# Performance work log

Measured on AMD Instinct MI355X. Metric: run time of the kernel, lower is better.

## Reference

```python
import jax, jax.numpy as jnp
import numpy as np

N = 16384
C = 128
F = 128

def setup_inputs() -> dict:
    key = jax.random.key(0)
    k1, k2, k3, k4 = jax.random.split(key, 4)
    X = jax.random.normal(k1, (N, C), dtype=jnp.float32)
    adj = jax.random.uniform(k2, (N, N), dtype=jnp.float32)
    W = jax.random.normal(k3, (C, F), dtype=jnp.float32) * 0.05
    b = jax.random.normal(k4, (F,), dtype=jnp.float32) * 0.05
    return {"X": X, "adj": adj, "W": W, "b": b}

def reference(X, adj, W, b):
    # adj_hat = adj + I (self-loops)
    adj_hat = adj + jnp.eye(adj.shape[0], dtype=adj.dtype)
    # D^{-1/2}: inverse of sqrt of the diagonal degree matrix == 1/sqrt(rowsum)
    d_inv_sqrt = 1.0 / jnp.sqrt(jnp.sum(adj_hat, axis=1))  # [N]
    # Symmetric normalization via row/col scaling (same math as D^-1/2 @ A @ D^-1/2)
    adj_norm = adj_hat * d_inv_sqrt[:, None] * d_inv_sqrt[None, :]
    # Feature transform first (N*C*F) then aggregate (N*N*F)
    out = adj_norm @ (X @ W) + b
    return jax.nn.relu(out)
```

## Files before the change

### kernel.cpp

```cpp
#include <hip/hip_runtime.h>
#include <hip/hip_bf16.h>

typedef __attribute__((ext_vector_type(8))) short short8;
typedef __attribute__((ext_vector_type(4))) float f32x4;

#define N_NODES 16384
#define FEAT 128
#define NTILES 256
#define KSPLIT 2
#define NT2 (NTILES / KSPLIT)

__device__ __forceinline__ short f2bf(float x) {
  union { float f; unsigned u; } v;
  v.f = x;
  unsigned r = v.u + 0x7fffu + ((v.u >> 16) & 1u);
  return (short)(r >> 16);
}

__global__ __launch_bounds__(256) void rowsum_kernel(
    const float* __restrict__ adj, float* __restrict__ dinv)
{
  const int row = blockIdx.x;
  const float4* p4 = (const float4*)(adj + (size_t)row * N_NODES);
  float s = 0.f;
  #pragma unroll 4
  for (int i = threadIdx.x; i < N_NODES / 4; i += 256) {
    float4 v = p4[i];
    s += (v.x + v.y) + (v.z + v.w);
  }
  #pragma unroll
  for (int off = 32; off > 0; off >>= 1) s += __shfl_down(s, off, 64);
  __shared__ float part[4];
  if ((threadIdx.x & 63) == 0) part[threadIdx.x >> 6] = s;
  __syncthreads();
  if (threadIdx.x == 0) {
    float tot = (part[0] + part[1]) + (part[2] + part[3]) + 1.0f;
    dinv[row] = rsqrtf(tot);
  }
}

__global__ __launch_bounds__(256) void xw_kernel(
    const float* __restrict__ X, const float* __restrict__ W,
    const float* __restrict__ dinv,
    __hip_bfloat16* __restrict__ Ypack)
{
  __shared__ __align__(16) float Ws[64][128];
  __shared__ __align__(16) float Xs[32][128];
  __shared__ __align__(16) short Ts[128][40];
  const int tid = threadIdx.x;
  const int row0 = blockIdx.x << 5;

  {
    const float4* Xg = (const float4*)(X + ((size_t)row0 << 7));
    float4* Xl = (float4*)&Xs[0][0];
    #pragma unroll
    for (int i = 0; i < 4; ++i) Xl[tid + (i << 8)] = Xg[tid + (i << 8)];
  }
  const int f  = tid & 127;
  const int rr = tid >> 7;
  float acc[16];
  #pragma unroll
  for (int k = 0; k < 16; ++k) acc[k] = 0.f;

  for (int cc = 0; cc < 2; ++cc) {
    __syncthreads();
    {
      const float4* Wg = (const float4*)(W + ((size_t)cc << 13));
      float4* Wl = (float4*)&Ws[0][0];
      #pragma unroll
      for (int i = 0; i < 8; ++i) Wl[tid + (i << 8)] = Wg[tid + (i << 8)];
    }
    __syncthreads();
    for (int c4 = 0; c4 < 16; ++c4) {
      const int cl = c4 << 2;
      const float w0 = Ws[cl + 0][f];
      const float w1 = Ws[cl + 1][f];
      const float w2 = Ws[cl + 2][f];
      const float w3 = Ws[cl + 3][f];
      const int cg = (cc << 6) + cl;
      #pragma unroll
      for (int k = 0; k < 16; ++k) {
        const float4 x = *(const float4*)&Xs[rr + (k << 1)][cg];
        acc[k] += x.x * w0 + x.y * w1 + x.z * w2 + x.w * w3;
      }
    }
  }
  #pragma unroll
  for (int k = 0; k < 16; ++k) {
    const int r = rr + (k << 1);
    const float dv = dinv[row0 + r];
    Ts[f][r] = f2bf(acc[k] * dv);
  }
  __syncthreads();
  {
    const int f2 = tid >> 1;
    const int h  = (tid & 1) << 4;
    const short8 v0 = *(const short8*)&Ts[f2][h];
    const short8 v1 = *(const short8*)&Ts[f2][h + 8];
    short* o = (short*)Ypack;
    *(short8*)(o + (size_t)(row0 + h) * FEAT + (f2 << 3))     = v0;
    *(short8*)(o + (size_t)(row0 + h + 8) * FEAT + (f2 << 3)) = v1;
  }
}

__global__ __launch_bounds__(512, 4) void spmm_kernel(
    const float* __restrict__ A,
    const __hip_bfloat16* __restrict__ Ypack,
    float* __restrict__ pws)
{
  __shared__ __align__(16) short As[2][4096];
  __shared__ __align__(16) short Bs[2][8192];

  const int tid = threadIdx.x;
  const int bid = blockIdx.x;
  const int mt  = bid & 255;
  const int s   = bid >> 8;
  const int row0 = mt << 6;

  const int ar  = tid >> 3;
  const int akg = tid & 7;
  const float* Ag = A + (size_t)(row0 + ar) * N_NODES + (s * NT2 << 6) + (akg << 3);
  const short* Yg = (const short*)Ypack + ((size_t)(s * NT2) << 13) + (tid << 4);

  const int wid  = tid >> 6;
  const int wm   = wid >> 1;
  const int wf   = wid & 1;
  const int lane = tid & 63;
  const int lm   = lane & 15;
  const int lkg  = (lane >> 4);
  const int myrow = (wm << 4) + lm;

  f32x4 acc[4];
  #pragma unroll
  for (int c = 0; c < 4; ++c) acc[c] = (f32x4){0.f, 0.f, 0.f, 0.f};

  float4 a0, a1;
  short8 y0, y1;

#define LOADT(T)                                                               \
  {                                                                            \
    const float* ap = Ag + ((T) << 6);                                         \
    a0 = *(const float4*)(ap);                                                 \
    a1 = *(const float4*)(ap + 4);                                             \
    const short* yp = Yg + ((T) << 13);                                        \
    y0 = *(const short8*)(yp);                                                 \
    y1 = *(const short8*)(yp + 8);                                             \
  }

#define STORET(T, P)                                                           \
  {                                                                            \
    if (s * NT2 + (T) == mt && (ar >> 3) == akg) {          \
      const int j = ar & 7;                                                    \
      a0.x += (j == 0) ? 1.f : 0.f;  a0.y += (j == 1) ? 1.f : 0.f;             \
      a0.z += (j == 2) ? 1.f : 0.f;  a0.w += (j == 3) ? 1.f : 0.f;             \
      a1.x += (j == 4) ? 1.f : 0.f;  a1.y += (j == 5) ? 1.f : 0.f;             \
      a1.z += (j == 6) ? 1.f : 0.f;  a1.w += (j == 7) ? 1.f : 0.f;             \
    }                                                                          \
    short8 av;                                                                 \
    av[0] = f2bf(a0.x); av[1] = f2bf(a0.y); av[2] = f2bf(a0.z);                \
    av[3] = f2bf(a0.w); av[4] = f2bf(a1.x); av[5] = f2bf(a1.y);                \
    av[6] = f2bf(a1.z); av[7] = f2bf(a1.w);                                    \
    *(short8*)&As[P][(akg << 9) + (ar << 3)] = av;                             \
    *(short8*)&Bs[P][tid << 4]       = y0;                                     \
    *(short8*)&Bs[P][(tid << 4) + 8] = y1;                                     \
  }

#define COMP(P)                                                                \
  {                                                                            \
    const short8 af0 = *(const short8*)&As[P][(lkg << 9) + (myrow << 3)];      \
    acc[0] = __builtin_amdgcn_mfma_f32_16x16x32_bf16(af0,                      \
        *(const short8*)&Bs[P][(lkg << 10) + (((wf << 6) + lm) << 3)], acc[0], 0, 0, 0); \
    acc[1] = __builtin_amdgcn_mfma_f32_16x16x32_bf16(af0,                      \
        *(const short8*)&Bs[P][(lkg << 10) + (((wf << 6) + 16 + lm) << 3)], acc[1], 0, 0, 0); \
    acc[2] = __builtin_amdgcn_mfma_f32_16x16x32_bf16(af0,                      \
        *(const short8*)&Bs[P][(lkg << 10) + (((wf << 6) + 32 + lm) << 3)], acc[2], 0, 0, 0); \
    acc[3] = __builtin_amdgcn_mfma_f32_16x16x32_bf16(af0,                      \
        *(const short8*)&Bs[P][(lkg << 10) + (((wf << 6) + 48 + lm) << 3)], acc[3], 0, 0, 0); \
    const short8 af1 = *(const short8*)&As[P][((4 + lkg) << 9) + (myrow << 3)];\
    acc[0] = __builtin_amdgcn_mfma_f32_16x16x32_bf16(af1,                      \
        *(const short8*)&Bs[P][((4 + lkg) << 10) + (((wf << 6) + lm) << 3)], acc[0], 0, 0, 0); \
    acc[1] = __builtin_amdgcn_mfma_f32_16x16x32_bf16(af1,                      \
        *(const short8*)&Bs[P][((4 + lkg) << 10) + (((wf << 6) + 16 + lm) << 3)], acc[1], 0, 0, 0); \
    acc[2] = __builtin_amdgcn_mfma_f32_16x16x32_bf16(af1,                      \
        *(const short8*)&Bs[P][((4 + lkg) << 10) + (((wf << 6) + 32 + lm) << 3)], acc[2], 0, 0, 0); \
    acc[3] = __builtin_amdgcn_mfma_f32_16x16x32_bf16(af1,                      \
        *(const short8*)&Bs[P][((4 + lkg) << 10) + (((wf << 6) + 48 + lm) << 3)], acc[3], 0, 0, 0); \
  }

  LOADT(0)
  STORET(0, 0)
  __syncthreads();

  int p = 0;
  for (int t = 0; t < NT2; ++t) {
    if (t + 1 < NT2) LOADT(t + 1)
    COMP(p)
    if (t + 1 < NT2) STORET(t + 1, p ^ 1)
    __syncthreads();
    p ^= 1;
  }

  float* pp = pws + ((size_t)(s * N_NODES + row0)) * FEAT;
  const int lr = (lane >> 4) << 2;
  #pragma unroll
  for (int c = 0; c < 4; ++c) {
    const int col = (wf << 6) + (c << 4) + lm;
    #pragma unroll
    for (int r = 0; r < 4; ++r) {
      pp[(size_t)((wm << 4) + lr + r) * FEAT + col] = acc[c][r];
    }
  }
#undef LOADT
#undef STORET
#undef COMP
}

__global__ __launch_bounds__(256) void reduce_kernel(
    const float* __restrict__ pws, const float* __restrict__ dinv,
    const float* __restrict__ bias, float* __restrict__ out)
{
  const int idx4 = blockIdx.x * 256 + threadIdx.x;
  const int row  = idx4 >> 5;
  const int f4   = idx4 & 31;
  const float4 p0 = ((const float4*)pws)[idx4];
  const float4 p1 = ((const float4*)pws)[idx4 + (N_NODES * FEAT / 4)];
  const float4 bv = ((const float4*)bias)[f4];
  const float  d  = dinv[row];
  float4 v;
  v.x = d * (p0.x + p1.x) + bv.x;
  v.y = d * (p0.y + p1.y) + bv.y;
  v.z = d * (p0.z + p1.z) + bv.z;
  v.w = d * (p0.w + p1.w) + bv.w;
  v.x = v.x > 0.f ? v.x : 0.f;
  v.y = v.y > 0.f ? v.y : 0.f;
  v.z = v.z > 0.f ? v.z : 0.f;
  v.w = v.w > 0.f ? v.w : 0.f;
  ((float4*)out)[idx4] = v;
}

extern "C" void kernel_launch(void* const* d_in, const int* in_sizes, int n_in,
                              void* d_out, int out_size, void* d_ws, size_t ws_size,
                              hipStream_t stream) {
  const float* X   = (const float*)d_in[0];
  const float* adj = (const float*)d_in[1];
  const float* W   = (const float*)d_in[2];
  const float* b   = (const float*)d_in[3];
  float* out = (float*)d_out;

  float* dinv           = (float*)d_ws;
  __hip_bfloat16* Ypack = (__hip_bfloat16*)((char*)d_ws + (1 << 16));
  float* pws            = (float*)((char*)d_ws + (1 << 16) + (1 << 22));

  rowsum_kernel<<<N_NODES, 256, 0, stream>>>(adj, dinv);
  xw_kernel<<<N_NODES / 32, 256, 0, stream>>>(X, W, dinv, Ypack);
  spmm_kernel<<<NTILES * KSPLIT, 512, 0, stream>>>(adj, Ypack, pws);
  reduce_kernel<<<N_NODES * FEAT / 4 / 256, 256, 0, stream>>>(pws, dinv, b, out);
}
```

Measured before the change: 409.6 us.

## Deepen global prefetch to two tiles and use lightweight barriers with MFMA priority

The main aggregation loop now keeps two register sets of global loads in flight, so tiles t+2 and t+3 are fetched while tile t is computed, instead of only one tile ahead. The loop is unrolled by two with fixed LDS buffers. __syncthreads is replaced by an lgkmcnt wait plus s_barrier, so the barrier no longer waits on outstanding global loads. s_setprio raises wave priority around the MFMA blocks. This aims to hide HBM latency on the streamed adjacency matrix, at the cost of more registers and possibly lower occupancy.

```diff
diff --git a/kernel.cpp b/kernel.cpp
--- a/kernel.cpp
+++ b/kernel.cpp
@@ -134,35 +134,35 @@
   #pragma unroll
   for (int c = 0; c < 4; ++c) acc[c] = (f32x4){0.f, 0.f, 0.f, 0.f};
 
-  float4 a0, a1;
-  short8 y0, y1;
-
-#define LOADT(T)                                                               \
+  float4 a0A, a1A, a0B, a1B;
+  short8 y0A, y1A, y0B, y1B;
+
+#define LOADT(T, A0_, A1_, Y0_, Y1_)                                           \
   {                                                                            \
-    const float* ap = Ag + ((T) << 6);                                         \
-    a0 = *(const float4*)(ap);                                                 \
-    a1 = *(const float4*)(ap + 4);                                             \
-    const short* yp = Yg + ((T) << 13);                                        \
-    y0 = *(const short8*)(yp);                                                 \
-    y1 = *(const short8*)(yp + 8);                                             \
-  }
-
-#define STORET(T, P)                                                           \
+    const float* ap = Ag + ((size_t)(T) << 6);                                 \
+    A0_ = *(const float4*)(ap);                                                \
+    A1_ = *(const float4*)(ap + 4);                                            \
+    const short* yp = Yg + ((size_t)(T) << 13);                                \
+    Y0_ = *(const short8*)(yp);                                                \
+    Y1_ = *(const short8*)(yp + 8);                                            \
+  }
+
+#define STORET(T, P, A0_, A1_, Y0_, Y1_)                                       \
   {                                                                            \
     if (s * NT2 + (T) == mt && (ar >> 3) == akg) {          \
       const int j = ar & 7;                                                    \
-      a0.x += (j == 0) ? 1.f : 0.f;  a0.y += (j == 1) ? 1.f : 0.f;             \
-      a0.z += (j == 2) ? 1.f : 0.f;  a0.w += (j == 3) ? 1.f : 0.f;             \
-      a1.x += (j == 4) ? 1.f : 0.f;  a1.y += (j == 5) ? 1.f : 0.f;             \
-      a1.z += (j == 6) ? 1.f : 0.f;  a1.w += (j == 7) ? 1.f : 0.f;             \
+      A0_.x += (j == 0) ? 1.f : 0.f;  A0_.y += (j == 1) ? 1.f : 0.f;           \
+      A0_.z += (j == 2) ? 1.f : 0.f;  A0_.w += (j == 3) ? 1.f : 0.f;           \
+      A1_.x += (j == 4) ? 1.f : 0.f;  A1_.y += (j == 5) ? 1.f : 0.f;           \
+      A1_.z += (j == 6) ? 1.f : 0.f;  A1_.w += (j == 7) ? 1.f : 0.f;           \
     }                                                                          \
     short8 av;                                                                 \
-    av[0] = f2bf(a0.x); av[1] = f2bf(a0.y); av[2] = f2bf(a0.z);                \
-    av[3] = f2bf(a0.w); av[4] = f2bf(a1.x); av[5] = f2bf(a1.y);                \
-    av[6] = f2bf(a1.z); av[7] = f2bf(a1.w);                                    \
+    av[0] = f2bf(A0_.x); av[1] = f2bf(A0_.y); av[2] = f2bf(A0_.z);             \
+    av[3] = f2bf(A0_.w); av[4] = f2bf(A1_.x); av[5] = f2bf(A1_.y);             \
+    av[6] = f2bf(A1_.z); av[7] = f2bf(A1_.w);                                  \
     *(short8*)&As[P][(akg << 9) + (ar << 3)] = av;                             \
-    *(short8*)&Bs[P][tid << 4]       = y0;                                     \
-    *(short8*)&Bs[P][(tid << 4) + 8] = y1;                                     \
+    *(short8*)&Bs[P][tid << 4]       = Y0_;                                    \
+    *(short8*)&Bs[P][(tid << 4) + 8] = Y1_;                                    \
   }
 
 #define COMP(P)                                                                \
@@ -187,17 +187,28 @@
         *(const short8*)&Bs[P][((4 + lkg) << 10) + (((wf << 6) + 48 + lm) << 3)], acc[3], 0, 0, 0); \
   }
 
-  LOADT(0)
-  STORET(0, 0)
-  __syncthreads();
-
-  int p = 0;
-  for (int t = 0; t < NT2; ++t) {
-    if (t + 1 < NT2) LOADT(t + 1)
-    COMP(p)
-    if (t + 1 < NT2) STORET(t + 1, p ^ 1)
-    __syncthreads();
-    p ^= 1;
+#define BAR()                                                                  \
+  asm volatile("s_waitcnt lgkmcnt(0)" ::: "memory");                           \
+  __builtin_amdgcn_s_barrier();
+
+  LOADT(0, a0A, a1A, y0A, y1A)
+  LOADT(1, a0B, a1B, y0B, y1B)
+  STORET(0, 0, a0A, a1A, y0A, y1A)
+  BAR()
+
+  for (int t = 0; t < NT2; t += 2) {
+    if (t + 2 < NT2) LOADT(t + 2, a0A, a1A, y0A, y1A)
+    __builtin_amdgcn_s_setprio(1);
+    COMP(0)
+    __builtin_amdgcn_s_setprio(0);
+    if (t + 1 < NT2) STORET(t + 1, 1, a0B, a1B, y0B, y1B)
+    BAR()
+    if (t + 3 < NT2) LOADT(t + 3, a0B, a1B, y0B, y1B)
+    __builtin_amdgcn_s_setprio(1);
+    COMP(1)
+    __builtin_amdgcn_s_setprio(0);
+    if (t + 2 < NT2) STORET(t + 2, 0, a0A, a1A, y0A, y1A)
+    BAR()
   }
 
   float* pp = pws + ((size_t)(s * N_NODES + row0)) * FEAT;
@@ -213,6 +224,7 @@
 #undef LOADT
 #undef STORET
 #undef COMP
+#undef BAR
 }
 
 __global__ __launch_bounds__(256) void reduce_kernel(
```

Result: no change. 409.2 us (-0.1%).

## Pre-pack adjacency to bf16 during rowsum and stream it into LDS asynchronously

Applied to the files above, without the earlier changes.

Merges the degree row-sum with a conversion of the fp32 adjacency into a tile-packed bf16 copy that includes the self-loop. The aggregation kernel then reads the packed bf16 tiles with direct global-to-LDS loads and triple buffering instead of converting fp32 in registers. This removes the conversion and register staging from the matmul loop and halves that kernel's read volume. In exchange it writes and re-reads a 512 MiB intermediate and needs a large workspace, so total memory traffic stays about the same.

```diff
diff --git a/kernel.cpp b/kernel.cpp
--- a/kernel.cpp
+++ b/kernel.cpp
@@ -17,26 +17,52 @@
   return (short)(r >> 16);
 }
 
-__global__ __launch_bounds__(256) void rowsum_kernel(
-    const float* __restrict__ adj, float* __restrict__ dinv)
-{
-  const int row = blockIdx.x;
-  const float4* p4 = (const float4*)(adj + (size_t)row * N_NODES);
+__global__ __launch_bounds__(256) void cvt_kernel(
+    const float* __restrict__ A, __hip_bfloat16* __restrict__ Apack,
+    float* __restrict__ psum)
+{
+  const int mt  = blockIdx.x & 255;
+  const int ks  = blockIdx.x >> 8;
+  const int tid = threadIdx.x;
+  const int r   = tid >> 2;
+  const int q   = tid & 3;
+  const int R   = (mt << 6) + r;
+  const float4* Arow = (const float4*)(A + (size_t)R * N_NODES) + (ks << 8);
+  short* Pb = (short*)Apack + ((size_t)mt << 20);
+
   float s = 0.f;
-  #pragma unroll 4
-  for (int i = threadIdx.x; i < N_NODES / 4; i += 256) {
-    float4 v = p4[i];
-    s += (v.x + v.y) + (v.z + v.w);
-  }
-  #pragma unroll
-  for (int off = 32; off > 0; off >>= 1) s += __shfl_down(s, off, 64);
-  __shared__ float part[4];
-  if ((threadIdx.x & 63) == 0) part[threadIdx.x >> 6] = s;
-  __syncthreads();
-  if (threadIdx.x == 0) {
-    float tot = (part[0] + part[1]) + (part[2] + part[3]) + 1.0f;
-    dinv[row] = rsqrtf(tot);
-  }
+  for (int tt = 0; tt < 16; ++tt) {
+    const int t = (ks << 4) + tt;
+    short* Pt = Pb + ((size_t)t << 12);
+    #pragma unroll
+    for (int i = 0; i < 4; ++i) {
+      const int idx = q + (i << 2);
+      float4 v = Arow[(tt << 4) + idx];
+      s += (v.x + v.y) + (v.z + v.w);
+      if (t == mt && idx == (r >> 2)) {
+        const int e = r & 3;
+        v.x += (e == 0) ? 1.f : 0.f;  v.y += (e == 1) ? 1.f : 0.f;
+        v.z += (e == 2) ? 1.f : 0.f;  v.w += (e == 3) ? 1.f : 0.f;
+      }
+      short4 o;
+      o.x = f2bf(v.x); o.y = f2bf(v.y); o.z = f2bf(v.z); o.w = f2bf(v.w);
+      *(short4*)&Pt[((idx >> 1) << 9) + (r << 3) + ((idx & 1) << 2)] = o;
+    }
+  }
+  s += __shfl_xor(s, 1, 64);
+  s += __shfl_xor(s, 2, 64);
+  if (q == 0) psum[((size_t)R << 4) + ks] = s;
+}
+
+__global__ __launch_bounds__(256) void dsum_kernel(
+    const float* __restrict__ psum, float* __restrict__ dinv)
+{
+  const int row = blockIdx.x * 256 + threadIdx.x;
+  const float4* p = (const float4*)(psum + ((size_t)row << 4));
+  const float4 a = p[0], b = p[1], c = p[2], d = p[3];
+  const float s = ((a.x + a.y) + (a.z + a.w)) + ((b.x + b.y) + (b.z + b.w))
+                + ((c.x + c.y) + (c.z + c.w)) + ((d.x + d.y) + (d.z + d.w));
+  dinv[row] = rsqrtf(s + 1.0f);
 }
 
 __global__ __launch_bounds__(256) void xw_kernel(
@@ -104,65 +130,43 @@
 }
 
 __global__ __launch_bounds__(512, 4) void spmm_kernel(
-    const float* __restrict__ A,
+    const __hip_bfloat16* __restrict__ Apack,
     const __hip_bfloat16* __restrict__ Ypack,
     float* __restrict__ pws)
 {
-  __shared__ __align__(16) short As[2][4096];
-  __shared__ __align__(16) short Bs[2][8192];
+  __shared__ __align__(16) short As[3][4096];
+  __shared__ __align__(16) short Bs[3][8192];
 
   const int tid = threadIdx.x;
-  const int bid = blockIdx.x;
-  const int mt  = bid & 255;
-  const int s   = bid >> 8;
+  const int mt  = blockIdx.x & 255;
+  const int s   = blockIdx.x >> 8;
   const int row0 = mt << 6;
-
-  const int ar  = tid >> 3;
-  const int akg = tid & 7;
-  const float* Ag = A + (size_t)(row0 + ar) * N_NODES + (s * NT2 << 6) + (akg << 3);
-  const short* Yg = (const short*)Ypack + ((size_t)(s * NT2) << 13) + (tid << 4);
-
   const int wid  = tid >> 6;
+  const int lane = tid & 63;
   const int wm   = wid >> 1;
   const int wf   = wid & 1;
-  const int lane = tid & 63;
   const int lm   = lane & 15;
-  const int lkg  = (lane >> 4);
+  const int lkg  = lane >> 4;
   const int myrow = (wm << 4) + lm;
 
-  f32x4 acc[4];
-  #pragma unroll
-  for (int c = 0; c < 4; ++c) acc[c] = (f32x4){0.f, 0.f, 0.f, 0.f};
-
-  float4 a0, a1;
-  short8 y0, y1;
-
-#define LOADT(T)                                                               \
+  const short* Ag = (const short*)Apack + ((size_t)mt << 20)
+                    + ((size_t)(s * NT2) << 12) + (tid << 3);
+  const short* Yg = (const short*)Ypack + ((size_t)(s * NT2) << 13) + (tid << 3);
+
+#define GLDS(T, P)                                                             \
   {                                                                            \
-    const float* ap = Ag + ((T) << 6);                                         \
-    a0 = *(const float4*)(ap);                                                 \
-    a1 = *(const float4*)(ap + 4);                                             \
-    const short* yp = Yg + ((T) << 13);                                        \
-    y0 = *(const short8*)(yp);                                                 \
-    y1 = *(const short8*)(yp + 8);                                             \
-  }
-
-#define STORET(T, P)                                                           \
-  {                                                                            \
-    if (s * NT2 + (T) == mt && (ar >> 3) == akg) {          \
-      const int j = ar & 7;                                                    \
-      a0.x += (j == 0) ? 1.f : 0.f;  a0.y += (j == 1) ? 1.f : 0.f;             \
-      a0.z += (j == 2) ? 1.f : 0.f;  a0.w += (j == 3) ? 1.f : 0.f;             \
-      a1.x += (j == 4) ? 1.f : 0.f;  a1.y += (j == 5) ? 1.f : 0.f;             \
-      a1.z += (j == 6) ? 1.f : 0.f;  a1.w += (j == 7) ? 1.f : 0.f;             \
-    }                                                                          \
-    short8 av;                                                                 \
-    av[0] = f2bf(a0.x); av[1] = f2bf(a0.y); av[2] = f2bf(a0.z);                \
-    av[3] = f2bf(a0.w); av[4] = f2bf(a1.x); av[5] = f2bf(a1.y);                \
-    av[6] = f2bf(a1.z); av[7] = f2bf(a1.w);                                    \
-    *(short8*)&As[P][(akg << 9) + (ar << 3)] = av;                             \
-    *(short8*)&Bs[P][tid << 4]       = y0;                                     \
-    *(short8*)&Bs[P][(tid << 4) + 8] = y1;                                     \
+    const short* as_ = Ag + ((size_t)(T) << 12);                               \
+    const short* ys_ = Yg + ((size_t)(T) << 13);                               \
+    __builtin_amdgcn_global_load_lds(                                          \
+        (const __attribute__((address_space(1))) void*)as_,                    \
+        (__attribute__((address_space(3))) void*)&As[P][wid << 9], 16, 0, 0);  \
+    __builtin_amdgcn_global_load_lds(                                          \
+        (const __attribute__((address_space(1))) void*)ys_,                    \
+        (__attribute__((address_space(3))) void*)&Bs[P][wid << 9], 16, 0, 0);  \
+    __builtin_amdgcn_global_load_lds(                                          \
+        (const __attribute__((address_space(1))) void*)(ys_ + 4096),           \
+        (__attribute__((address_space(3))) void*)&Bs[P][4096 + (wid << 9)],    \
+        16, 0, 0);                                                             \
   }
 
 #define COMP(P)                                                                \
@@ -187,17 +191,29 @@
         *(const short8*)&Bs[P][((4 + lkg) << 10) + (((wf << 6) + 48 + lm) << 3)], acc[3], 0, 0, 0); \
   }
 
-  LOADT(0)
-  STORET(0, 0)
-  __syncthreads();
+  f32x4 acc[4];
+  #pragma unroll
+  for (int c = 0; c < 4; ++c) acc[c] = (f32x4){0.f, 0.f, 0.f, 0.f};
+
+  GLDS(0, 0)
+  GLDS(1, 1)
+  asm volatile("s_waitcnt vmcnt(3)" ::: "memory");
+  __builtin_amdgcn_s_barrier();
 
   int p = 0;
   for (int t = 0; t < NT2; ++t) {
-    if (t + 1 < NT2) LOADT(t + 1)
+    __builtin_amdgcn_s_setprio(1);
     COMP(p)
-    if (t + 1 < NT2) STORET(t + 1, p ^ 1)
-    __syncthreads();
-    p ^= 1;
+    __builtin_amdgcn_s_setprio(0);
+    if (t + 2 < NT2) {
+      int np = p + 2; if (np >= 3) np -= 3;
+      GLDS(t + 2, np)
+      asm volatile("s_waitcnt vmcnt(3)" ::: "memory");
+    } else {
+      asm volatile("s_waitcnt vmcnt(0)" ::: "memory");
+    }
+    __builtin_amdgcn_s_barrier();
+    ++p; if (p >= 3) p -= 3;
   }
 
   float* pp = pws + ((size_t)(s * N_NODES + row0)) * FEAT;
@@ -210,8 +226,7 @@
       pp[(size_t)((wm << 4) + lr + r) * FEAT + col] = acc[c][r];
     }
   }
-#undef LOADT
-#undef STORET
+#undef GLDS
 #undef COMP
 }
 
@@ -248,11 +263,14 @@
   float* out = (float*)d_out;
 
   float* dinv           = (float*)d_ws;
-  __hip_bfloat16* Ypack = (__hip_bfloat16*)((char*)d_ws + (1 << 16));
-  float* pws            = (float*)((char*)d_ws + (1 << 16) + (1 << 22));
-
-  rowsum_kernel<<<N_NODES, 256, 0, stream>>>(adj, dinv);
+  float* psum           = (float*)((char*)d_ws + (1 << 20));
+  __hip_bfloat16* Ypack = (__hip_bfloat16*)((char*)d_ws + (2 << 20));
+  float* pws            = (float*)((char*)d_ws + (8 << 20));
+  __hip_bfloat16* Apack = (__hip_bfloat16*)((char*)d_ws + (32u << 20));
+
+  cvt_kernel<<<256 * 16, 256, 0, stream>>>(adj, Apack, psum);
+  dsum_kernel<<<N_NODES / 256, 256, 0, stream>>>(psum, dinv);
   xw_kernel<<<N_NODES / 32, 256, 0, stream>>>(X, W, dinv, Ypack);
-  spmm_kernel<<<NTILES * KSPLIT, 512, 0, stream>>>(adj, Ypack, pws);
+  spmm_kernel<<<NTILES * KSPLIT, 512, 0, stream>>>(Apack, Ypack, pws);
   reduce_kernel<<<N_NODES * FEAT / 4 / 256, 256, 0, stream>>>(pws, dinv, b, out);
 }
```

Measured after the change: 490.5 us. 19.7% more time.
